# Kernel tuning notes

Hardware: AMD Instinct MI355X
Metric: run time of the kernel (lower is better)

The kernel has to match this reference:

```python
import jax, jax.numpy as jnp
import numpy as np

B, D, H, L, T = 4096, 256, 512, 2, 45


def _lstm_cell(x, h, c, W_ih, W_hh, b_ih, b_hh):
    # PyTorch LSTM gate order: i, f, g, o
    gates = x @ W_ih + h @ W_hh + b_ih + b_hh  # [B, 4H]
    i, f, g, o = jnp.split(gates, 4, axis=-1)
    i = jax.nn.sigmoid(i)
    f = jax.nn.sigmoid(f)
    g = jnp.tanh(g)
    o = jax.nn.sigmoid(o)
    c_new = f * c + i * g
    h_new = o * jnp.tanh(c_new)
    return h_new, c_new


def setup_inputs() -> dict:
    key = jax.random.key(0)
    ks = jax.random.split(key, 32)
    s = 0.02
    inp = {
        "encoder_feat": jax.random.normal(ks[0], (B, D), jnp.float32),
        "context": jax.random.normal(ks[1], (B, D), jnp.float32),
        "initial_intent": jax.random.uniform(ks[2], (B, 1), jnp.float32),
        # hidden/cell init linears: d_model -> H*L (stored [in, out])
        "Wh_init": jax.random.normal(ks[3], (D, H * L), jnp.float32) * s,
        "bh_init": jnp.zeros((H * L,), jnp.float32),
        "Wc_init": jax.random.normal(ks[4], (D, H * L), jnp.float32) * s,
        "bc_init": jnp.zeros((H * L,), jnp.float32),
        # LSTM layer 0: input size 1 + d_model
        "W_ih0": jax.random.normal(ks[5], (1 + D, 4 * H), jnp.float32) * s,
        "W_hh0": jax.random.normal(ks[6], (H, 4 * H), jnp.float32) * s,
        "b_ih0": jnp.zeros((4 * H,), jnp.float32),
        "b_hh0": jnp.zeros((4 * H,), jnp.float32),
        # LSTM layer 1: input size H
        "W_ih1": jax.random.normal(ks[7], (H, 4 * H), jnp.float32) * s,
        "W_hh1": jax.random.normal(ks[8], (H, 4 * H), jnp.float32) * s,
        "b_ih1": jnp.zeros((4 * H,), jnp.float32),
        "b_hh1": jnp.zeros((4 * H,), jnp.float32),
        # output_proj: H -> 32 -> 1
        "Wo1": jax.random.normal(ks[9], (H, 32), jnp.float32) * s,
        "bo1": jnp.zeros((32,), jnp.float32),
        "Wo2": jax.random.normal(ks[10], (32, 1), jnp.float32) * s,
        "bo2": jnp.zeros((1,), jnp.float32),
        # global_intent_head: H -> 32 -> 1
        "Wg1": jax.random.normal(ks[11], (H, 32), jnp.float32) * s,
        "bg1": jnp.zeros((32,), jnp.float32),
        "Wg2": jax.random.normal(ks[12], (32, 1), jnp.float32) * s,
        "bg2": jnp.zeros((1,), jnp.float32),
    }
    return inp


def reference(encoder_feat, context, initial_intent,
              Wh_init, bh_init, Wc_init, bc_init,
              W_ih0, W_hh0, b_ih0, b_hh0,
              W_ih1, W_hh1, b_ih1, b_hh1,
              Wo1, bo1, Wo2, bo2, Wg1, bg1, Wg2, bg2):
    # init hidden/cell: [B, L*H] -> [B, L, H]; layer-major slices
    h_init = (encoder_feat @ Wh_init + bh_init).reshape(B, L, H)
    c_init = (encoder_feat @ Wc_init + bc_init).reshape(B, L, H)
    h0, h1 = h_init[:, 0], h_init[:, 1]
    c0, c1 = c_init[:, 0], c_init[:, 1]

    def step(carry, _):
        h0, c0, h1, c1, intent = carry
        x = jnp.concatenate([intent, context], axis=-1)  # [B, 1+D]
        h0n, c0n = _lstm_cell(x, h0, c0, W_ih0, W_hh0, b_ih0, b_hh0)
        h1n, c1n = _lstm_cell(h0n, h1, c1, W_ih1, W_hh1, b_ih1, b_hh1)
        logit = jax.nn.relu(h1n @ Wo1 + bo1) @ Wo2 + bo2  # [B, 1]
        intent_new = jax.nn.sigmoid(logit)
        return (h0n, c0n, h1n, c1n, intent_new), intent_new

    carry0 = (h0, c0, h1, c1, initial_intent)
    (h0, c0, h1, c1, _), ys = jax.lax.scan(step, carry0, None, length=T)
    step_intents = jnp.transpose(ys, (1, 0, 2))  # [B, T, 1]
    global_logit = jax.nn.relu(h1 @ Wg1 + bg1) @ Wg2 + bg2
    global_intent = jax.nn.sigmoid(global_logit)  # [B, 1]
    return step_intents, global_intent
```

## Files before the change

### kernel.cpp

```cpp
#include <hip/hip_runtime.h>
#include <hip/hip_bf16.h>

#define Bsz 4096
#define Dsz 256
#define Hsz 512
#define Tsz 45

typedef __attribute__((ext_vector_type(8))) short short8;
typedef __attribute__((ext_vector_type(4))) float f32x4;
typedef __attribute__((ext_vector_type(4))) unsigned short us4;
using bf16 = __hip_bfloat16;

__device__ __forceinline__ float sigf(float x)   { return 1.0f / (1.0f + __expf(-x)); }
__device__ __forceinline__ float tanhft(float x) { return 1.0f - 2.0f / (__expf(2.0f * x) + 1.0f); }
__device__ __forceinline__ float b2f(unsigned short u) { return __uint_as_float((unsigned)u << 16); }

__device__ __forceinline__ void gload16(const void* g, void* l) {
    __builtin_amdgcn_global_load_lds((const __attribute__((address_space(1))) void*)g,
                                     (__attribute__((address_space(3))) void*)l, 16, 0, 0);
}

__global__ void k_conv(const float* __restrict__ ef,   const float* __restrict__ ctx,
                       const float* __restrict__ Whi,  const float* __restrict__ Wci,
                       const float* __restrict__ Wih0, const float* __restrict__ Whh0,
                       const float* __restrict__ Wih1, const float* __restrict__ Whh1,
                       const float* __restrict__ Wo1,  const float* __restrict__ Wg1,
                       bf16* __restrict__ efb,  bf16* __restrict__ ctxb,
                       bf16* __restrict__ Wit,  bf16* __restrict__ Wt0,
                       bf16* __restrict__ Wt1,  bf16* __restrict__ Wo1t,
                       bf16* __restrict__ Wg1t)
{
    size_t tid = (size_t)blockIdx.x * blockDim.x + threadIdx.x;
    size_t gsz = (size_t)gridDim.x * blockDim.x;
    for (size_t i = tid; i < (size_t)Bsz * Dsz; i += gsz) {
        efb[i]  = __float2bfloat16(ef[i]);
        ctxb[i] = __float2bfloat16(ctx[i]);
    }
    for (size_t i = tid; i < 2048ull * 512; i += gsz) {
        size_t n = i >> 9, k = i & 511;
        Wt0[i] = __float2bfloat16(Whh0[k * 2048 + n]);
    }
    for (size_t i = tid; i < 2048ull * 1024; i += gsz) {
        size_t n = i >> 10, k = i & 1023;
        Wt1[i] = __float2bfloat16(k < 512 ? Wih1[k * 2048 + n] : Whh1[(k - 512) * 2048 + n]);
    }
    for (size_t i = tid; i < 32ull * 512; i += gsz) {
        size_t c = i >> 9, k = i & 511;
        Wo1t[i] = __float2bfloat16(Wo1[k * 32 + c]);
        Wg1t[i] = __float2bfloat16(Wg1[k * 32 + c]);
    }
    for (size_t i = tid; i < 4096ull * 256; i += gsz) {
        size_t n = i >> 8, k = i & 255;
        float v = (n < 1024) ? Whi[k * 1024 + n]
                : (n < 2048) ? Wci[k * 1024 + (n - 1024)]
                             : Wih0[(1 + k) * 2048 + (n - 2048)];
        Wit[i] = __float2bfloat16(v);
    }
}

__global__ void __launch_bounds__(256)
k_init(const bf16* __restrict__ efb, const bf16* __restrict__ ctxb,
       const bf16* __restrict__ Wit,
       const float* __restrict__ bh,  const float* __restrict__ bc,
       const float* __restrict__ bi0, const float* __restrict__ bh0,
       bf16* __restrict__ h0, bf16* __restrict__ h1,
       float* __restrict__ c0, float* __restrict__ c1,
       bf16* __restrict__ ctxg)
{
    const int t = threadIdx.x, lane = t & 63, w = t >> 6;
    const int wr = w >> 1, wc = w & 1;
    const int lq = lane >> 4, ln = lane & 15;
    const int m0 = blockIdx.x * 128, n0 = blockIdx.y * 64;
    const bf16* A = (n0 < 2048) ? efb : ctxb;

    f32x4 zero = {0.f, 0.f, 0.f, 0.f};
    f32x4 acc[4][2];
#pragma unroll
    for (int r = 0; r < 4; ++r)
#pragma unroll
        for (int c = 0; c < 2; ++c) acc[r][c] = zero;

    for (int k0 = 0; k0 < 256; k0 += 32) {
        short8 af[4];
#pragma unroll
        for (int r = 0; r < 4; ++r)
            af[r] = *(const short8*)(A + (size_t)(m0 + wr * 64 + r * 16 + ln) * 256 + k0 + lq * 8);
#pragma unroll
        for (int c = 0; c < 2; ++c) {
            short8 bv = *(const short8*)(Wit + (size_t)(n0 + wc * 32 + c * 16 + ln) * 256 + k0 + lq * 8);
#pragma unroll
            for (int r = 0; r < 4; ++r)
                acc[r][c] = __builtin_amdgcn_mfma_f32_16x16x32_bf16(af[r], bv, acc[r][c], 0, 0, 0);
        }
    }
#pragma unroll
    for (int r = 0; r < 4; ++r)
#pragma unroll
        for (int c = 0; c < 2; ++c)
#pragma unroll
            for (int e = 0; e < 4; ++e) {
                int b = m0 + wr * 64 + r * 16 + lq * 4 + e;
                int n = n0 + wc * 32 + c * 16 + ln;
                float v = acc[r][c][e];
                if (n < 1024) {
                    v += bh[n];
                    if (n < 512) h0[(size_t)b * 512 + n]       = __float2bfloat16(v);
                    else         h1[(size_t)b * 512 + n - 512] = __float2bfloat16(v);
                } else if (n < 2048) {
                    int m = n - 1024; v += bc[m];
                    if (m < 512) c0[(size_t)b * 512 + m]       = v;
                    else         c1[(size_t)b * 512 + m - 512] = v;
                } else {
                    int j = n - 2048;
                    ctxg[(size_t)b * 2048 + (j & 511) * 4 + (j >> 9)] =
                        __float2bfloat16(v + bi0[j] + bh0[j]);
                }
            }
}

__device__ __forceinline__ void intent_head(
    const bf16* __restrict__ h, const bf16* __restrict__ W1t,
    const float* __restrict__ b1, const float* __restrict__ W2, float b2s,
    int m0, float* sitp, float* outp, int ostride)
{
    const int t = threadIdx.x, lane = t & 63, w = t >> 6;
    const int lq = lane >> 4, ln = lane & 15;
    f32x4 zero = {0.f, 0.f, 0.f, 0.f};
    f32x4 acc[2][2];
#pragma unroll
    for (int r = 0; r < 2; ++r)
#pragma unroll
        for (int c = 0; c < 2; ++c) acc[r][c] = zero;

#pragma unroll
    for (int k0 = 0; k0 < 512; k0 += 32) {
        short8 av[2], bv[2];
#pragma unroll
        for (int r = 0; r < 2; ++r)
            av[r] = *(const short8*)(h + (size_t)(m0 + w * 32 + r * 16 + ln) * 512 + k0 + lq * 8);
#pragma unroll
        for (int c = 0; c < 2; ++c)
            bv[c] = *(const short8*)(W1t + (size_t)(c * 16 + ln) * 512 + k0 + lq * 8);
#pragma unroll
        for (int r = 0; r < 2; ++r)
#pragma unroll
            for (int c = 0; c < 2; ++c)
                acc[r][c] = __builtin_amdgcn_mfma_f32_16x16x32_bf16(av[r], bv[c], acc[r][c], 0, 0, 0);
    }
#pragma unroll
    for (int r = 0; r < 2; ++r)
#pragma unroll
        for (int e = 0; e < 4; ++e) {
            float v = 0.f;
#pragma unroll
            for (int c = 0; c < 2; ++c) {
                int col = c * 16 + ln;
                v += fmaxf(acc[r][c][e] + b1[col], 0.f) * W2[col];
            }
            v += __shfl_xor(v, 1);
            v += __shfl_xor(v, 2);
            v += __shfl_xor(v, 4);
            v += __shfl_xor(v, 8);
            int row = w * 32 + r * 16 + lq * 4 + e;
            if (ln == 0) {
                float p = sigf(v + b2s);
                if (sitp) sitp[row] = p;
                if (outp) outp[(size_t)(m0 + row) * ostride] = p;
            }
        }
}

template <int L0>
__device__ __forceinline__ void stage(const bf16* __restrict__ hA, const bf16* __restrict__ hB,
                                      const bf16* __restrict__ Wt,
                                      int m0, int j0, int k0, bf16* Ab, bf16* Bb, int t)
{
    constexpr int KW = L0 ? 512 : 1024;
#pragma unroll
    for (int i = 0; i < 4; ++i) {
        int f = i * 256 + t;
        int row = f >> 3, slot = f & 7;
        int kk = k0 + ((slot ^ (row & 7)) << 3);
        const bf16* src;
        if (L0) src = hA + (size_t)(m0 + row) * Hsz + kk;
        else    src = (kk < 512) ? hA + (size_t)(m0 + row) * Hsz + kk
                                 : hB + (size_t)(m0 + row) * Hsz + (kk - 512);
        gload16(src, (char*)Ab + (size_t)f * 16);
    }
#pragma unroll
    for (int i = 0; i < 4; ++i) {
        int f = i * 256 + t;
        int brow = f >> 3, slot = f & 7;
        int g = brow >> 5, n = brow & 31;
        int kc = slot ^ (brow & 7);
        gload16(Wt + (size_t)(g * 512 + j0 + n) * KW + k0 + kc * 8, (char*)Bb + (size_t)f * 16);
    }
}

template <int L0>
__global__ void __launch_bounds__(256, 2)
k_gates(const bf16* __restrict__ hA, const bf16* __restrict__ hB,
        const bf16* __restrict__ Wt,
        const bf16* __restrict__ ctxg, const float* __restrict__ ii,
        const bf16* __restrict__ h1prev,
        const float* __restrict__ w0row,
        const float* __restrict__ b1, const float* __restrict__ b2,
        const bf16* __restrict__ Wo1t, const float* __restrict__ bo1,
        const float* __restrict__ Wo2, const float* __restrict__ bo2,
        float* __restrict__ cbuf, bf16* __restrict__ hout,
        float* __restrict__ outp, int step)
{
    constexpr int KW = L0 ? 512 : 1024;
    constexpr int NT = KW / 64;
    __shared__ __align__(16) char lds[65536];
    bf16* A0 = (bf16*)lds;
    bf16* A1 = (bf16*)(lds + 16384);
    bf16* B0 = (bf16*)(lds + 32768);
    bf16* B1 = (bf16*)(lds + 49152);
    float* sitp = (float*)(lds + 49152);

    const int t = threadIdx.x, lane = t & 63, w = t >> 6;
    const int wr = w >> 1, wc = w & 1, lq = lane >> 4, ln = lane & 15;
    const int j0 = blockIdx.x * 32, m0 = blockIdx.y * 128;

    stage<L0>(hA, hB, Wt, m0, j0, 0, A0, B0, t);

    float sreg[16];
    if (L0) {
        if (step == 0) {
            if (t < 128) sitp[t] = ii[m0 + t];
        } else {
            intent_head(h1prev, Wo1t, bo1, Wo2, bo2[0], m0, sitp,
                        (blockIdx.x == 0) ? outp + (step - 1) : nullptr, Tsz);
        }
        __syncthreads();
#pragma unroll
        for (int r = 0; r < 4; ++r)
#pragma unroll
            for (int e = 0; e < 4; ++e)
                sreg[r * 4 + e] = sitp[wr * 64 + r * 16 + lq * 4 + e];
        __syncthreads();
    } else {
        __syncthreads();
    }

    f32x4 zero = {0.f, 0.f, 0.f, 0.f};
    f32x4 acc[4][4];
#pragma unroll
    for (int g = 0; g < 4; ++g)
#pragma unroll
        for (int r = 0; r < 4; ++r) acc[g][r] = zero;

#pragma unroll 2
    for (int kt = 0; kt < NT; ++kt) {
        if (kt + 1 < NT)
            stage<L0>(hA, hB, Wt, m0, j0, (kt + 1) * 64,
                      (kt & 1) ? A0 : A1, (kt & 1) ? B0 : B1, t);
        const bf16* Ab = (kt & 1) ? A1 : A0;
        const bf16* Bb = (kt & 1) ? B1 : B0;
#pragma unroll
        for (int kk2 = 0; kk2 < 2; ++kk2) {
            short8 af[4], bfr[4];
#pragma unroll
            for (int r = 0; r < 4; ++r) {
                int row = wr * 64 + r * 16 + ln;
                int slot = (kk2 * 4 + lq) ^ (row & 7);
                af[r] = *(const short8*)(Ab + ((size_t)row * 8 + slot) * 8);
            }
#pragma unroll
            for (int g = 0; g < 4; ++g) {
                int brow = g * 32 + wc * 16 + ln;
                int slot = (kk2 * 4 + lq) ^ (brow & 7);
                bfr[g] = *(const short8*)(Bb + ((size_t)brow * 8 + slot) * 8);
            }
#pragma unroll
            for (int g = 0; g < 4; ++g)
#pragma unroll
                for (int r = 0; r < 4; ++r)
                    acc[g][r] = __builtin_amdgcn_mfma_f32_16x16x32_bf16(af[r], bfr[g], acc[g][r], 0, 0, 0);
        }
        if (kt + 1 < NT) __syncthreads();
    }

    const int jl = j0 + wc * 16 + ln;
    float addc[4];
#pragma unroll
    for (int g = 0; g < 4; ++g)
        addc[g] = L0 ? w0row[g * 512 + jl] : (b1[g * 512 + jl] + b2[g * 512 + jl]);

#pragma unroll
    for (int r = 0; r < 4; ++r)
#pragma unroll
        for (int e = 0; e < 4; ++e) {
            int b = m0 + wr * 64 + r * 16 + lq * 4 + e;
            float pre[4];
#pragma unroll
            for (int g = 0; g < 4; ++g) pre[g] = acc[g][r][e];
            if (L0) {
                float it = sreg[r * 4 + e];
                us4 cg = *(const us4*)((const unsigned short*)ctxg + (size_t)b * 2048 + jl * 4);
#pragma unroll
                for (int g = 0; g < 4; ++g) pre[g] += b2f(cg[g]) + it * addc[g];
            } else {
#pragma unroll
                for (int g = 0; g < 4; ++g) pre[g] += addc[g];
            }
            float ig = sigf(pre[0]), fg = sigf(pre[1]);
            float gg = tanhft(pre[2]), og = sigf(pre[3]);
            size_t idx = (size_t)b * Hsz + jl;
            float cn = fg * cbuf[idx] + ig * gg;
            cbuf[idx] = cn;
            hout[idx] = __float2bfloat16(og * tanhft(cn));
        }
}

__global__ void __launch_bounds__(256)
k_intent(const bf16* __restrict__ h, const bf16* __restrict__ W1t,
         const float* __restrict__ bias1, const float* __restrict__ W2,
         const float* __restrict__ bias2,
         float* __restrict__ outp, int ostride)
{
    intent_head(h, W1t, bias1, W2, bias2[0], blockIdx.x * 128, nullptr, outp, ostride);
}

extern "C" void kernel_launch(void* const* d_in, const int* in_sizes, int n_in,
                              void* d_out, int out_size, void* d_ws, size_t ws_size,
                              hipStream_t stream)
{
    const float* ef   = (const float*)d_in[0];
    const float* ctx  = (const float*)d_in[1];
    const float* ii   = (const float*)d_in[2];
    const float* Whi  = (const float*)d_in[3];
    const float* bh   = (const float*)d_in[4];
    const float* Wci  = (const float*)d_in[5];
    const float* bc   = (const float*)d_in[6];
    const float* Wih0 = (const float*)d_in[7];
    const float* Whh0 = (const float*)d_in[8];
    const float* bi0  = (const float*)d_in[9];
    const float* bh0  = (const float*)d_in[10];
    const float* Wih1 = (const float*)d_in[11];
    const float* Whh1 = (const float*)d_in[12];
    const float* bi1  = (const float*)d_in[13];
    const float* bh1  = (const float*)d_in[14];
    const float* Wo1  = (const float*)d_in[15];
    const float* bo1  = (const float*)d_in[16];
    const float* Wo2  = (const float*)d_in[17];
    const float* bo2  = (const float*)d_in[18];
    const float* Wg1  = (const float*)d_in[19];
    const float* bg1  = (const float*)d_in[20];
    const float* Wg2  = (const float*)d_in[21];
    const float* bg2  = (const float*)d_in[22];
    float* out = (float*)d_out;

    char* ws = (char*)d_ws;
    size_t off = 0;
    auto take = [&](size_t bytes) -> char* {
        char* pp = ws + off;
        off += (bytes + 255) & ~(size_t)255;
        return pp;
    };
    bf16* Wt0    = (bf16*)take(2048ull * 512 * 2);
    bf16* Wt1    = (bf16*)take(2048ull * 1024 * 2);
    bf16* Wo1t   = (bf16*)take(32ull * 512 * 2);
    bf16* Wg1t   = (bf16*)take(32ull * 512 * 2);
    bf16* Wit    = (bf16*)take(4096ull * 256 * 2);
    bf16* efb    = (bf16*)take((size_t)Bsz * Dsz * 2);
    bf16* ctxb   = (bf16*)take((size_t)Bsz * Dsz * 2);
    bf16* h0x    = (bf16*)take((size_t)Bsz * Hsz * 2);
    bf16* h0y    = (bf16*)take((size_t)Bsz * Hsz * 2);
    bf16* h1x    = (bf16*)take((size_t)Bsz * Hsz * 2);
    bf16* h1y    = (bf16*)take((size_t)Bsz * Hsz * 2);
    float* c0    = (float*)take((size_t)Bsz * Hsz * 4);
    float* c1    = (float*)take((size_t)Bsz * Hsz * 4);
    bf16* ctxg   = (bf16*)take((size_t)Bsz * 2048 * 2);
    (void)ws_size; (void)in_sizes; (void)n_in; (void)out_size;

    k_conv<<<2048, 256, 0, stream>>>(ef, ctx, Whi, Wci, Wih0, Whh0, Wih1, Whh1, Wo1, Wg1,
                                     efb, ctxb, Wit, Wt0, Wt1, Wo1t, Wg1t);
    k_init<<<dim3(32, 64), 256, 0, stream>>>(efb, ctxb, Wit, bh, bc, bi0, bh0,
                                             h0x, h1x, c0, c1, ctxg);

    for (int s = 0; s < Tsz; ++s) {
        int p = s & 1;
        const bf16* h0in  = p ? h0y : h0x;
        bf16*       h0out = p ? h0x : h0y;
        const bf16* h1in  = p ? h1y : h1x;
        bf16*       h1out = p ? h1x : h1y;
        k_gates<1><<<dim3(16, 32), 256, 0, stream>>>(
            h0in, nullptr, Wt0, ctxg, ii, h1in, Wih0, nullptr, nullptr,
            Wo1t, bo1, Wo2, bo2, c0, h0out, out, s);
        k_gates<0><<<dim3(16, 32), 256, 0, stream>>>(
            h0out, h1in, Wt1, nullptr, nullptr, nullptr, nullptr, bi1, bh1,
            nullptr, nullptr, nullptr, nullptr, c1, h1out, nullptr, s);
    }
    k_intent<<<32, 256, 0, stream>>>(h1y, Wo1t, bo1, Wo2, bo2, out + 44, Tsz);
    k_intent<<<32, 256, 0, stream>>>(h1y, Wg1t, bg1, Wg2, bg2, out + (size_t)Bsz * Tsz, 1);
}
```

Before: 2.757 ms.

## Halve gate GEMM M-tile and K-step to raise occupancy and grid size

Shrinks the per-block batch tile from 128 to 64 rows and the K step from 64 to 32, cutting LDS use from 64KB to about 24KB and raising launch bounds to 4 blocks per CU. The grid doubles to 1024 blocks per step, and the swizzle, staging and intent-head mapping are reworked for the smaller tiles. The goal is more parallelism and latency hiding on the 256-CU part. In exchange, weight tiles are reused across fewer rows, there are twice as many syncs per K, and the intent head is recomputed by twice as many blocks.

Result: slower. 3.428 ms (+24.3%).

```diff
diff --git a/kernel.cpp b/kernel.cpp
--- a/kernel.cpp
+++ b/kernel.cpp
@@ -126,48 +126,38 @@
     const int t = threadIdx.x, lane = t & 63, w = t >> 6;
     const int lq = lane >> 4, ln = lane & 15;
     f32x4 zero = {0.f, 0.f, 0.f, 0.f};
-    f32x4 acc[2][2];
-#pragma unroll
-    for (int r = 0; r < 2; ++r)
-#pragma unroll
-        for (int c = 0; c < 2; ++c) acc[r][c] = zero;
+    f32x4 acc[2];
+#pragma unroll
+    for (int c = 0; c < 2; ++c) acc[c] = zero;
 
 #pragma unroll
     for (int k0 = 0; k0 < 512; k0 += 32) {
-        short8 av[2], bv[2];
-#pragma unroll
-        for (int r = 0; r < 2; ++r)
-            av[r] = *(const short8*)(h + (size_t)(m0 + w * 32 + r * 16 + ln) * 512 + k0 + lq * 8);
-#pragma unroll
-        for (int c = 0; c < 2; ++c)
-            bv[c] = *(const short8*)(W1t + (size_t)(c * 16 + ln) * 512 + k0 + lq * 8);
-#pragma unroll
-        for (int r = 0; r < 2; ++r)
-#pragma unroll
-            for (int c = 0; c < 2; ++c)
-                acc[r][c] = __builtin_amdgcn_mfma_f32_16x16x32_bf16(av[r], bv[c], acc[r][c], 0, 0, 0);
-    }
-#pragma unroll
-    for (int r = 0; r < 2; ++r)
-#pragma unroll
-        for (int e = 0; e < 4; ++e) {
-            float v = 0.f;
-#pragma unroll
-            for (int c = 0; c < 2; ++c) {
-                int col = c * 16 + ln;
-                v += fmaxf(acc[r][c][e] + b1[col], 0.f) * W2[col];
-            }
-            v += __shfl_xor(v, 1);
-            v += __shfl_xor(v, 2);
-            v += __shfl_xor(v, 4);
-            v += __shfl_xor(v, 8);
-            int row = w * 32 + r * 16 + lq * 4 + e;
-            if (ln == 0) {
-                float p = sigf(v + b2s);
-                if (sitp) sitp[row] = p;
-                if (outp) outp[(size_t)(m0 + row) * ostride] = p;
-            }
-        }
+        short8 av = *(const short8*)(h + (size_t)(m0 + w * 16 + ln) * 512 + k0 + lq * 8);
+#pragma unroll
+        for (int c = 0; c < 2; ++c) {
+            short8 bv = *(const short8*)(W1t + (size_t)(c * 16 + ln) * 512 + k0 + lq * 8);
+            acc[c] = __builtin_amdgcn_mfma_f32_16x16x32_bf16(av, bv, acc[c], 0, 0, 0);
+        }
+    }
+#pragma unroll
+    for (int e = 0; e < 4; ++e) {
+        float v = 0.f;
+#pragma unroll
+        for (int c = 0; c < 2; ++c) {
+            int col = c * 16 + ln;
+            v += fmaxf(acc[c][e] + b1[col], 0.f) * W2[col];
+        }
+        v += __shfl_xor(v, 1);
+        v += __shfl_xor(v, 2);
+        v += __shfl_xor(v, 4);
+        v += __shfl_xor(v, 8);
+        int row = w * 16 + lq * 4 + e;
+        if (ln == 0) {
+            float p = sigf(v + b2s);
+            if (sitp) sitp[row] = p;
+            if (outp) outp[(size_t)(m0 + row) * ostride] = p;
+        }
+    }
 }
 
 template <int L0>
@@ -176,29 +166,51 @@
                                       int m0, int j0, int k0, bf16* Ab, bf16* Bb, int t)
 {
     constexpr int KW = L0 ? 512 : 1024;
-#pragma unroll
-    for (int i = 0; i < 4; ++i) {
-        int f = i * 256 + t;
-        int row = f >> 3, slot = f & 7;
-        int kk = k0 + ((slot ^ (row & 7)) << 3);
+    {
+        int row = t >> 2, slot = t & 3;
+        int kk = k0 + ((slot ^ ((row >> 1) & 3)) << 3);
         const bf16* src;
         if (L0) src = hA + (size_t)(m0 + row) * Hsz + kk;
         else    src = (kk < 512) ? hA + (size_t)(m0 + row) * Hsz + kk
                                  : hB + (size_t)(m0 + row) * Hsz + (kk - 512);
-        gload16(src, (char*)Ab + (size_t)f * 16);
-    }
-#pragma unroll
-    for (int i = 0; i < 4; ++i) {
+        gload16(src, (char*)Ab + (size_t)t * 16);
+    }
+#pragma unroll
+    for (int i = 0; i < 2; ++i) {
         int f = i * 256 + t;
-        int brow = f >> 3, slot = f & 7;
-        int g = brow >> 5, n = brow & 31;
-        int kc = slot ^ (brow & 7);
-        gload16(Wt + (size_t)(g * 512 + j0 + n) * KW + k0 + kc * 8, (char*)Bb + (size_t)f * 16);
-    }
+        int brow = f >> 2, slot = f & 3;
+        int kc = slot ^ ((brow >> 1) & 3);
+        gload16(Wt + (size_t)((brow >> 5) * 512 + j0 + (brow & 31)) * KW + k0 + kc * 8,
+                (char*)Bb + (size_t)f * 16);
+    }
+}
+
+__device__ __forceinline__ void mfma_tile(const bf16* Ab, const bf16* Bb,
+                                          int wr, int wc, int lq, int ln,
+                                          f32x4 (&acc)[4][2])
+{
+    short8 af[2], bfr[4];
+#pragma unroll
+    for (int r = 0; r < 2; ++r) {
+        int row = wr * 32 + r * 16 + ln;
+        int slot = lq ^ ((row >> 1) & 3);
+        af[r] = *(const short8*)(Ab + ((size_t)row * 4 + slot) * 8);
+    }
+#pragma unroll
+    for (int g = 0; g < 4; ++g) {
+        int brow = g * 32 + wc * 16 + ln;
+        int slot = lq ^ ((brow >> 1) & 3);
+        bfr[g] = *(const short8*)(Bb + ((size_t)brow * 4 + slot) * 8);
+    }
+#pragma unroll
+    for (int g = 0; g < 4; ++g)
+#pragma unroll
+        for (int r = 0; r < 2; ++r)
+            acc[g][r] = __builtin_amdgcn_mfma_f32_16x16x32_bf16(af[r], bfr[g], acc[g][r], 0, 0, 0);
 }
 
 template <int L0>
-__global__ void __launch_bounds__(256, 2)
+__global__ void __launch_bounds__(256, 4)
 k_gates(const bf16* __restrict__ hA, const bf16* __restrict__ hB,
         const bf16* __restrict__ Wt,
         const bf16* __restrict__ ctxg, const float* __restrict__ ii,
@@ -211,74 +223,51 @@
         float* __restrict__ outp, int step)
 {
     constexpr int KW = L0 ? 512 : 1024;
-    constexpr int NT = KW / 64;
-    __shared__ __align__(16) char lds[65536];
+    constexpr int NT = KW / 32;
+    __shared__ __align__(16) char lds[24576];
+    __shared__ float sitp[64];
     bf16* A0 = (bf16*)lds;
-    bf16* A1 = (bf16*)(lds + 16384);
-    bf16* B0 = (bf16*)(lds + 32768);
-    bf16* B1 = (bf16*)(lds + 49152);
-    float* sitp = (float*)(lds + 49152);
+    bf16* A1 = (bf16*)(lds + 4096);
+    bf16* B0 = (bf16*)(lds + 8192);
+    bf16* B1 = (bf16*)(lds + 16384);
 
     const int t = threadIdx.x, lane = t & 63, w = t >> 6;
     const int wr = w >> 1, wc = w & 1, lq = lane >> 4, ln = lane & 15;
-    const int j0 = blockIdx.x * 32, m0 = blockIdx.y * 128;
+    const int j0 = blockIdx.x * 32, m0 = blockIdx.y * 64;
 
     stage<L0>(hA, hB, Wt, m0, j0, 0, A0, B0, t);
 
-    float sreg[16];
+    float sreg[8];
     if (L0) {
         if (step == 0) {
-            if (t < 128) sitp[t] = ii[m0 + t];
+            if (t < 64) sitp[t] = ii[m0 + t];
         } else {
             intent_head(h1prev, Wo1t, bo1, Wo2, bo2[0], m0, sitp,
                         (blockIdx.x == 0) ? outp + (step - 1) : nullptr, Tsz);
         }
-        __syncthreads();
-#pragma unroll
-        for (int r = 0; r < 4; ++r)
+    }
+    __syncthreads();
+    if (L0) {
+#pragma unroll
+        for (int r = 0; r < 2; ++r)
 #pragma unroll
             for (int e = 0; e < 4; ++e)
-                sreg[r * 4 + e] = sitp[wr * 64 + r * 16 + lq * 4 + e];
-        __syncthreads();
-    } else {
-        __syncthreads();
+                sreg[r * 4 + e] = sitp[wr * 32 + r * 16 + lq * 4 + e];
     }
 
     f32x4 zero = {0.f, 0.f, 0.f, 0.f};
-    f32x4 acc[4][4];
+    f32x4 acc[4][2];
 #pragma unroll
     for (int g = 0; g < 4; ++g)
 #pragma unroll
-        for (int r = 0; r < 4; ++r) acc[g][r] = zero;
+        for (int r = 0; r < 2; ++r) acc[g][r] = zero;
 
 #pragma unroll 2
     for (int kt = 0; kt < NT; ++kt) {
         if (kt + 1 < NT)
-            stage<L0>(hA, hB, Wt, m0, j0, (kt + 1) * 64,
+            stage<L0>(hA, hB, Wt, m0, j0, (kt + 1) * 32,
                       (kt & 1) ? A0 : A1, (kt & 1) ? B0 : B1, t);
-        const bf16* Ab = (kt & 1) ? A1 : A0;
-        const bf16* Bb = (kt & 1) ? B1 : B0;
-#pragma unroll
-        for (int kk2 = 0; kk2 < 2; ++kk2) {
-            short8 af[4], bfr[4];
-#pragma unroll
-            for (int r = 0; r < 4; ++r) {
-                int row = wr * 64 + r * 16 + ln;
-                int slot = (kk2 * 4 + lq) ^ (row & 7);
-                af[r] = *(const short8*)(Ab + ((size_t)row * 8 + slot) * 8);
-            }
-#pragma unroll
-            for (int g = 0; g < 4; ++g) {
-                int brow = g * 32 + wc * 16 + ln;
-                int slot = (kk2 * 4 + lq) ^ (brow & 7);
-                bfr[g] = *(const short8*)(Bb + ((size_t)brow * 8 + slot) * 8);
-            }
-#pragma unroll
-            for (int g = 0; g < 4; ++g)
-#pragma unroll
-                for (int r = 0; r < 4; ++r)
-                    acc[g][r] = __builtin_amdgcn_mfma_f32_16x16x32_bf16(af[r], bfr[g], acc[g][r], 0, 0, 0);
-        }
+        mfma_tile((kt & 1) ? A1 : A0, (kt & 1) ? B1 : B0, wr, wc, lq, ln, acc);
         if (kt + 1 < NT) __syncthreads();
     }
 
@@ -289,10 +278,10 @@
         addc[g] = L0 ? w0row[g * 512 + jl] : (b1[g * 512 + jl] + b2[g * 512 + jl]);
 
 #pragma unroll
-    for (int r = 0; r < 4; ++r)
+    for (int r = 0; r < 2; ++r)
 #pragma unroll
         for (int e = 0; e < 4; ++e) {
-            int b = m0 + wr * 64 + r * 16 + lq * 4 + e;
+            int b = m0 + wr * 32 + r * 16 + lq * 4 + e;
             float pre[4];
 #pragma unroll
             for (int g = 0; g < 4; ++g) pre[g] = acc[g][r][e];
@@ -320,7 +309,7 @@
          const float* __restrict__ bias2,
          float* __restrict__ outp, int ostride)
 {
-    intent_head(h, W1t, bias1, W2, bias2[0], blockIdx.x * 128, nullptr, outp, ostride);
+    intent_head(h, W1t, bias1, W2, bias2[0], blockIdx.x * 64, nullptr, outp, ostride);
 }
 
 extern "C" void kernel_launch(void* const* d_in, const int* in_sizes, int n_in,
@@ -386,13 +375,13 @@
         bf16*       h0out = p ? h0x : h0y;
         const bf16* h1in  = p ? h1y : h1x;
         bf16*       h1out = p ? h1x : h1y;
-        k_gates<1><<<dim3(16, 32), 256, 0, stream>>>(
+        k_gates<1><<<dim3(16, 64), 256, 0, stream>>>(
             h0in, nullptr, Wt0, ctxg, ii, h1in, Wih0, nullptr, nullptr,
             Wo1t, bo1, Wo2, bo2, c0, h0out, out, s);
-        k_gates<0><<<dim3(16, 32), 256, 0, stream>>>(
+        k_gates<0><<<dim3(16, 64), 256, 0, stream>>>(
             h0out, h1in, Wt1, nullptr, nullptr, nullptr, nullptr, bi1, bh1,
             nullptr, nullptr, nullptr, nullptr, c1, h1out, nullptr, s);
     }
-    k_intent<<<32, 256, 0, stream>>>(h1y, Wo1t, bo1, Wo2, bo2, out + 44, Tsz);
-    k_intent<<<32, 256, 0, stream>>>(h1y, Wg1t, bg1, Wg2, bg2, out + (size_t)Bsz * Tsz, 1);
-}
+    k_intent<<<64, 256, 0, stream>>>(h1y, Wo1t, bo1, Wo2, bo2, out + 44, Tsz);
+    k_intent<<<64, 256, 0, stream>>>(h1y, Wg1t, bg1, Wg2, bg2, out + (size_t)Bsz * Tsz, 1);
+}
```

## Deepen gate GEMM pipeline to 4-stage K=32 ring with vmcnt waits and XCD-aware block mapping

Applied to the files above, without the earlier changes.

Reworks the k_gates GEMM main loop from a double-buffered K=64 tile into a four-slot ring of K=32 tiles. Three tiles are kept in flight, and each step waits with explicit s_waitcnt vmcnt plus a raw barrier instead of __syncthreads. The LDS swizzle changes to match the 4-slot rows. The launch grid becomes a flat 1D grid whose block index is remapped so each XCD gets contiguous j-blocks, aiming for better L2 reuse of weights. The goal is to hide global-to-LDS latency and improve cache locality, at the cost of relying on hand-counted vmcnt values and a single barrier per step, which is fragile.

Result: slower. 2.965 ms (+7.5%).

```diff
diff --git a/kernel.cpp b/kernel.cpp
--- a/kernel.cpp
+++ b/kernel.cpp
@@ -173,29 +173,57 @@
 template <int L0>
 __device__ __forceinline__ void stage(const bf16* __restrict__ hA, const bf16* __restrict__ hB,
                                       const bf16* __restrict__ Wt,
-                                      int m0, int j0, int k0, bf16* Ab, bf16* Bb, int t)
+                                      int m0, int j0, int k0, char* buf, int t)
 {
     constexpr int KW = L0 ? 512 : 1024;
 #pragma unroll
-    for (int i = 0; i < 4; ++i) {
+    for (int i = 0; i < 2; ++i) {
         int f = i * 256 + t;
-        int row = f >> 3, slot = f & 7;
-        int kk = k0 + ((slot ^ (row & 7)) << 3);
+        int row = f >> 2, slot = f & 3;
+        int kk = k0 + ((slot ^ ((row >> 1) & 3)) << 3);
         const bf16* src;
         if (L0) src = hA + (size_t)(m0 + row) * Hsz + kk;
         else    src = (kk < 512) ? hA + (size_t)(m0 + row) * Hsz + kk
                                  : hB + (size_t)(m0 + row) * Hsz + (kk - 512);
-        gload16(src, (char*)Ab + (size_t)f * 16);
-    }
-#pragma unroll
-    for (int i = 0; i < 4; ++i) {
+        gload16(src, buf + (size_t)f * 16);
+    }
+#pragma unroll
+    for (int i = 0; i < 2; ++i) {
         int f = i * 256 + t;
-        int brow = f >> 3, slot = f & 7;
-        int g = brow >> 5, n = brow & 31;
-        int kc = slot ^ (brow & 7);
-        gload16(Wt + (size_t)(g * 512 + j0 + n) * KW + k0 + kc * 8, (char*)Bb + (size_t)f * 16);
-    }
-}
+        int brow = f >> 2, slot = f & 3;
+        int kc = slot ^ ((brow >> 1) & 3);
+        gload16(Wt + (size_t)((brow >> 5) * 512 + j0 + (brow & 31)) * KW + k0 + kc * 8,
+                buf + 8192 + (size_t)f * 16);
+    }
+}
+
+__device__ __forceinline__ void mfma_tile(const char* buf,
+                                          int wr, int wc, int lq, int ln,
+                                          f32x4 (&acc)[4][4])
+{
+    const bf16* Ab = (const bf16*)buf;
+    const bf16* Bb = (const bf16*)(buf + 8192);
+    short8 af[4], bfr[4];
+#pragma unroll
+    for (int r = 0; r < 4; ++r) {
+        int row = wr * 64 + r * 16 + ln;
+        int slot = lq ^ ((row >> 1) & 3);
+        af[r] = *(const short8*)(Ab + ((size_t)row * 4 + slot) * 8);
+    }
+#pragma unroll
+    for (int g = 0; g < 4; ++g) {
+        int brow = g * 32 + wc * 16 + ln;
+        int slot = lq ^ ((brow >> 1) & 3);
+        bfr[g] = *(const short8*)(Bb + ((size_t)brow * 4 + slot) * 8);
+    }
+#pragma unroll
+    for (int g = 0; g < 4; ++g)
+#pragma unroll
+        for (int r = 0; r < 4; ++r)
+            acc[g][r] = __builtin_amdgcn_mfma_f32_16x16x32_bf16(af[r], bfr[g], acc[g][r], 0, 0, 0);
+}
+
+#define WAIT_VM(N) asm volatile("s_waitcnt vmcnt(" #N ")" ::: "memory")
 
 template <int L0>
 __global__ void __launch_bounds__(256, 2)
@@ -211,19 +239,20 @@
         float* __restrict__ outp, int step)
 {
     constexpr int KW = L0 ? 512 : 1024;
-    constexpr int NT = KW / 64;
+    constexpr int NT = KW / 32;
     __shared__ __align__(16) char lds[65536];
-    bf16* A0 = (bf16*)lds;
-    bf16* A1 = (bf16*)(lds + 16384);
-    bf16* B0 = (bf16*)(lds + 32768);
-    bf16* B1 = (bf16*)(lds + 49152);
-    float* sitp = (float*)(lds + 49152);
+    __shared__ float sitp[128];
 
     const int t = threadIdx.x, lane = t & 63, w = t >> 6;
     const int wr = w >> 1, wc = w & 1, lq = lane >> 4, ln = lane & 15;
-    const int j0 = blockIdx.x * 32, m0 = blockIdx.y * 128;
-
-    stage<L0>(hA, hB, Wt, m0, j0, 0, A0, B0, t);
+    const int bid = blockIdx.x;
+    const int xcd = bid & 7, idx = bid >> 3;
+    const int jblk = xcd * 2 + (idx >> 5), mblk = idx & 31;
+    const int j0 = jblk * 32, m0 = mblk * 128;
+
+    stage<L0>(hA, hB, Wt, m0, j0, 0,  lds,         t);
+    stage<L0>(hA, hB, Wt, m0, j0, 32, lds + 16384, t);
+    stage<L0>(hA, hB, Wt, m0, j0, 64, lds + 32768, t);
 
     float sreg[16];
     if (L0) {
@@ -231,17 +260,15 @@
             if (t < 128) sitp[t] = ii[m0 + t];
         } else {
             intent_head(h1prev, Wo1t, bo1, Wo2, bo2[0], m0, sitp,
-                        (blockIdx.x == 0) ? outp + (step - 1) : nullptr, Tsz);
+                        (jblk == 0) ? outp + (step - 1) : nullptr, Tsz);
         }
-        __syncthreads();
+        asm volatile("s_waitcnt lgkmcnt(0)" ::: "memory");
+        __builtin_amdgcn_s_barrier();
 #pragma unroll
         for (int r = 0; r < 4; ++r)
 #pragma unroll
             for (int e = 0; e < 4; ++e)
                 sreg[r * 4 + e] = sitp[wr * 64 + r * 16 + lq * 4 + e];
-        __syncthreads();
-    } else {
-        __syncthreads();
     }
 
     f32x4 zero = {0.f, 0.f, 0.f, 0.f};
@@ -251,36 +278,22 @@
 #pragma unroll
         for (int r = 0; r < 4; ++r) acc[g][r] = zero;
 
-#pragma unroll 2
-    for (int kt = 0; kt < NT; ++kt) {
-        if (kt + 1 < NT)
-            stage<L0>(hA, hB, Wt, m0, j0, (kt + 1) * 64,
-                      (kt & 1) ? A0 : A1, (kt & 1) ? B0 : B1, t);
-        const bf16* Ab = (kt & 1) ? A1 : A0;
-        const bf16* Bb = (kt & 1) ? B1 : B0;
-#pragma unroll
-        for (int kk2 = 0; kk2 < 2; ++kk2) {
-            short8 af[4], bfr[4];
-#pragma unroll
-            for (int r = 0; r < 4; ++r) {
-                int row = wr * 64 + r * 16 + ln;
-                int slot = (kk2 * 4 + lq) ^ (row & 7);
-                af[r] = *(const short8*)(Ab + ((size_t)row * 8 + slot) * 8);
-            }
-#pragma unroll
-            for (int g = 0; g < 4; ++g) {
-                int brow = g * 32 + wc * 16 + ln;
-                int slot = (kk2 * 4 + lq) ^ (brow & 7);
-                bfr[g] = *(const short8*)(Bb + ((size_t)brow * 8 + slot) * 8);
-            }
-#pragma unroll
-            for (int g = 0; g < 4; ++g)
-#pragma unroll
-                for (int r = 0; r < 4; ++r)
-                    acc[g][r] = __builtin_amdgcn_mfma_f32_16x16x32_bf16(af[r], bfr[g], acc[g][r], 0, 0, 0);
-        }
-        if (kt + 1 < NT) __syncthreads();
-    }
+#pragma unroll 4
+    for (int kt = 0; kt < NT - 3; ++kt) {
+        WAIT_VM(8);
+        __builtin_amdgcn_s_barrier();
+        mfma_tile(lds + (size_t)(kt & 3) * 16384, wr, wc, lq, ln, acc);
+        stage<L0>(hA, hB, Wt, m0, j0, (kt + 3) * 32, lds + (size_t)((kt + 3) & 3) * 16384, t);
+    }
+    WAIT_VM(8);
+    __builtin_amdgcn_s_barrier();
+    mfma_tile(lds + (size_t)((NT - 3) & 3) * 16384, wr, wc, lq, ln, acc);
+    WAIT_VM(4);
+    __builtin_amdgcn_s_barrier();
+    mfma_tile(lds + (size_t)((NT - 2) & 3) * 16384, wr, wc, lq, ln, acc);
+    WAIT_VM(0);
+    __builtin_amdgcn_s_barrier();
+    mfma_tile(lds + (size_t)((NT - 1) & 3) * 16384, wr, wc, lq, ln, acc);
 
     const int jl = j0 + wc * 16 + ln;
     float addc[4];
@@ -307,10 +320,10 @@
             }
             float ig = sigf(pre[0]), fg = sigf(pre[1]);
             float gg = tanhft(pre[2]), og = sigf(pre[3]);
-            size_t idx = (size_t)b * Hsz + jl;
-            float cn = fg * cbuf[idx] + ig * gg;
-            cbuf[idx] = cn;
-            hout[idx] = __float2bfloat16(og * tanhft(cn));
+            size_t idxb = (size_t)b * Hsz + jl;
+            float cn = fg * cbuf[idxb] + ig * gg;
+            cbuf[idxb] = cn;
+            hout[idxb] = __float2bfloat16(og * tanhft(cn));
         }
 }
 
@@ -386,10 +399,10 @@
         bf16*       h0out = p ? h0x : h0y;
         const bf16* h1in  = p ? h1y : h1x;
         bf16*       h1out = p ? h1x : h1y;
-        k_gates<1><<<dim3(16, 32), 256, 0, stream>>>(
+        k_gates<1><<<512, 256, 0, stream>>>(
             h0in, nullptr, Wt0, ctxg, ii, h1in, Wih0, nullptr, nullptr,
             Wo1t, bo1, Wo2, bo2, c0, h0out, out, s);
-        k_gates<0><<<dim3(16, 32), 256, 0, stream>>>(
+        k_gates<0><<<512, 256, 0, stream>>>(
             h0out, h1in, Wt1, nullptr, nullptr, nullptr, nullptr, bi1, bh1,
             nullptr, nullptr, nullptr, nullptr, c1, h1out, nullptr, s);
     }
```
